# Performance work log

Hardware: AMD Instinct MI355X
Metric: run time of the kernel (lower is better)

## Reference

```python
import jax, jax.numpy as jnp
import numpy as np

N, M, H, C = 20000, 20000, 32, 128
KP_EXTENT = 0.6
EPS = 1e-5


def _kpconv(q_pts, s_pts, neighb_inds, x, kernel_points, weights):
    """Rigid KPConv, linear influence, 'sum' aggregation, Predator-style density norm."""
    # shadow point / shadow feature padding (index M is the shadow slot)
    s_pad = jnp.concatenate([s_pts, jnp.full((1, 3), 1e6, s_pts.dtype)], axis=0)
    x_pad = jnp.concatenate([x, jnp.zeros((1, x.shape[1]), x.dtype)], axis=0)
    neighbors = s_pad[neighb_inds] - q_pts[:, None, :]              # [N,H,3]
    diff = neighbors[:, :, None, :] - kernel_points[None, None]      # [N,H,K,3]
    sq = jnp.sum(diff * diff, axis=-1)                               # [N,H,K]
    dist = jnp.sqrt(jnp.maximum(sq, 1e-12))
    all_weights = jnp.clip(1.0 - dist / KP_EXTENT, 0.0, None)        # linear KP influence
    neighb_x = x_pad[neighb_inds]                                    # [N,H,C]
    weighted = jnp.einsum('nhk,nhc->nkc', all_weights, neighb_x)     # [N,K,C]
    out = jnp.einsum('nkc,kcd->nd', weighted, weights)               # [N,D]
    # density normalization by number of valid neighbors
    feat_sum = jnp.sum(neighb_x, axis=-1)                            # [N,H]
    n_num = jnp.maximum(jnp.sum(feat_sum > 0.0, axis=-1), 1)         # [N]
    return out / n_num[:, None].astype(out.dtype)


def _segment_norm(x, len0):
    """Per-cloud (instance) normalization over stacked points, 2 clouds, no affine."""
    n = x.shape[0]
    seg = (jnp.arange(n) >= len0).astype(jnp.int32)                  # [N] in {0,1}
    onehot = jax.nn.one_hot(seg, 2, dtype=x.dtype)                   # [N,2]
    cnt = jnp.maximum(onehot.sum(axis=0), 1.0)                       # [2]
    mean = (onehot.T @ x) / cnt[:, None]                             # [2,C]
    var = (onehot.T @ (x * x)) / cnt[:, None] - mean * mean          # [2,C]
    return (x - mean[seg]) * jax.lax.rsqrt(var[seg] + EPS)


def _batchnorm1d(x, gamma, beta):
    mean = jnp.mean(x, axis=0)
    var = jnp.mean(x * x, axis=0) - mean * mean                      # biased, as torch BN
    return (x - mean) * jax.lax.rsqrt(var + EPS) * gamma + beta


def _rand_kernel_points(key, k, radius):
    pts = jax.random.normal(key, (k, 3), dtype=jnp.float32)
    pts = pts / jnp.linalg.norm(pts, axis=1, keepdims=True)
    r = jax.random.uniform(jax.random.fold_in(key, 1), (k, 1)) ** (1.0 / 3.0)
    return pts * r * radius


def setup_inputs() -> dict:
    key = jax.random.key(0)
    ks = jax.random.split(key, 10)
    D = C // 2  # 64, per-branch out channels
    q_pts = jax.random.uniform(ks[0], (N, 3), dtype=jnp.float32)
    s_pts = jax.random.uniform(ks[1], (M, 3), dtype=jnp.float32)
    neighb_inds = jax.random.randint(ks[2], (N, H), 0, M)
    x = jax.random.normal(ks[3], (M, C), dtype=jnp.float32)
    stack_lengths_post = jnp.array([N // 2, N - N // 2], dtype=jnp.int32)
    kp_mini = _rand_kernel_points(ks[4], 7, 1.0 * 1.5)               # radius * 1.5
    w_mini = jax.random.normal(ks[5], (7, C, D), dtype=jnp.float32) * (1.0 / np.sqrt(C))
    kp_mid = _rand_kernel_points(ks[6], 13, 1.0)                      # radius
    w_mid = jax.random.normal(ks[7], (13, C, D), dtype=jnp.float32) * (1.0 / np.sqrt(C))
    w_midmini = jax.random.normal(ks[8], (D, D), dtype=jnp.float32) * (1.0 / np.sqrt(D))
    w_final = jax.random.normal(ks[9], (C, C), dtype=jnp.float32) * (1.0 / np.sqrt(C))
    gamma_final = jnp.ones((C,), jnp.float32)
    beta_final = jnp.zeros((C,), jnp.float32)
    return dict(q_pts=q_pts, s_pts=s_pts, neighb_inds=neighb_inds, x=x,
                stack_lengths_post=stack_lengths_post,
                kp_mini=kp_mini, w_mini=w_mini, kp_mid=kp_mid, w_mid=w_mid,
                w_midmini=w_midmini, w_final=w_final,
                gamma_final=gamma_final, beta_final=beta_final)


def reference(q_pts, s_pts, neighb_inds, x, stack_lengths_post,
              kp_mini, w_mini, kp_mid, w_mid, w_midmini, w_final,
              gamma_final, beta_final):
    len0 = stack_lengths_post[0]
    x1 = _kpconv(q_pts, s_pts, neighb_inds, x, kp_mini, w_mini)      # [N, C//2]
    x1 = _segment_norm(x1, len0)
    x2 = _kpconv(q_pts, s_pts, neighb_inds, x, kp_mid, w_mid)        # [N, C//2]
    x2 = _segment_norm(x2, len0)
    x2 = (x1 + x2) @ w_midmini.T                                     # nn.Linear(bias=False)
    xc = jnp.concatenate([x1, x2], axis=1)                           # [N, C]
    out = xc @ w_final.T
    out = _batchnorm1d(out, gamma_final, beta_final)
    return jax.nn.relu(out)
```

## Files before the change

### kernel.cpp

```cpp
#include <hip/hip_runtime.h>
#include <math.h>

#define NQ 20000
#define MS 20000
#define HN 32
#define CH 128
#define DH 64
#define KTOT 20
#define KMINI 7
#define EPSN 1e-5f
#define KDIM 2560
#define NKT 80
#define NMT 1250
#define KT_Y1 28

#define OFF_ROWSUM 0
#define OFF_Y1     20480
#define OFF_Y2     (OFF_Y1 + NQ*DH)
#define OFF_SEG    (OFF_Y2 + NQ*DH)
#define OFF_SEGSUM (OFF_SEG + 512)
#define OFF_BNSUM  (OFF_SEGSUM + 512)
#define OFF_BNSQ   (OFF_BNSUM + 128)
#define OFF_OUTPRE (OFF_BNSQ + 128)
#define OFF_WSWZ   (OFF_OUTPRE + NQ*CH)
#define OFF_P      (OFF_WSWZ + 163840)
#define OFF_CFRAG  (OFF_P + NQ*KDIM/2)
#define TOT_FLOATS (OFF_CFRAG + 8192)

typedef __attribute__((ext_vector_type(8))) short bf16x8;
typedef __attribute__((ext_vector_type(4))) float f32x4;
typedef __attribute__((ext_vector_type(4))) unsigned short us4;

static __device__ inline unsigned short f2bf(float f) {
    unsigned int u = __float_as_uint(f);
    unsigned int r = (u + 0x7fffu + ((u >> 16) & 1u)) >> 16;
    return (unsigned short)r;
}

__global__ __launch_bounds__(256) void k_prep(
    const float* __restrict__ x, float* __restrict__ rowsum,
    const float* __restrict__ w_mini, const float* __restrict__ w_mid,
    const float* __restrict__ w_midmini, const float* __restrict__ w_final,
    unsigned short* __restrict__ wswz, unsigned short* __restrict__ cfrag)
{
    if (blockIdx.x < 5000) {
        int row = blockIdx.x * 4 + (threadIdx.x >> 6);
        int lane = threadIdx.x & 63;
        if (row >= MS) return;
        double s = (double)x[row * CH + lane] + (double)x[row * CH + 64 + lane];
        #pragma unroll
        for (int off = 32; off > 0; off >>= 1) s += __shfl_down(s, off, 64);
        if (lane == 0) rowsum[row] = (float)s;
    } else if (blockIdx.x < 6280) {
        int gid = (blockIdx.x - 5000) * 256 + threadIdx.x;
        if (gid >= NKT * 8 * 512) return;
        int j = gid & 7;
        int l = (gid >> 3) & 63;
        int ntkt = gid >> 9;
        int nt = ntkt & 7;
        int kt = ntkt >> 3;
        int kg = kt * 32 + ((l >> 4) << 3) + j;
        int d  = nt * 16 + (l & 15);
        int k = kg >> 7, c = kg & 127;
        float v = 0.0f;
        if (k < KMINI && d < DH)        v = w_mini[((size_t)k * CH + c) * DH + d];
        else if (k >= KMINI && d >= DH) v = w_mid[((size_t)(k - KMINI) * CH + c) * DH + (d - DH)];
        wswz[gid] = f2bf(v);
    } else {
        int b2 = blockIdx.x - 6280;
        int kt = b2 >> 3, nt = b2 & 7;
        for (int e = threadIdx.x; e < 512; e += 256) {
            int l = e >> 3, j = e & 7;
            int i = kt * 32 + ((l >> 4) << 3) + j;
            int jcol = nt * 16 + (l & 15);
            const float* wfr = &w_final[(size_t)jcol * 128 + 64];
            int ec = i & 63;
            float dsum = 0.f;
            #pragma unroll 8
            for (int dd = 0; dd < 64; ++dd)
                dsum += w_midmini[dd * 64 + ec] * wfr[dd];
            float cv = dsum + ((i < 64) ? w_final[(size_t)jcol * 128 + i] : 0.f);
            cfrag[(size_t)(kt * 8 + nt) * 512 + e] = f2bf(cv);
        }
    }
}

__global__ __launch_bounds__(256) void k_gather(
    const float* __restrict__ q_pts, const float* __restrict__ s_pts,
    const int* __restrict__ inds, const float* __restrict__ x,
    const float* __restrict__ kp_mini, const float* __restrict__ kp_mid,
    const float* __restrict__ rowsum,
    unsigned short* __restrict__ P)
{
    __shared__ __align__(16) float kpts[KTOT][3];
    __shared__ __align__(16) float nb[256][3];
    __shared__ int   nidx[256];
    __shared__ int   vcnt[8];
    __shared__ float winv[8];
    __shared__ __align__(16) float wts[8][HN][KTOT];

    const int t = threadIdx.x;
    const int n0 = blockIdx.x * 8;

    if (t < KTOT * 3) {
        int k = t / 3, j = t % 3;
        kpts[k][j] = (k < KMINI) ? kp_mini[k * 3 + j] : kp_mid[(k - KMINI) * 3 + j];
    }
    if (t < 8) vcnt[t] = 0;
    __syncthreads();

    {
        int r = t >> 5, h = t & 31;
        int n = n0 + r;
        int idx = inds[n * HN + h];
        nidx[t] = idx;
        float qx = q_pts[n * 3 + 0], qy = q_pts[n * 3 + 1], qz = q_pts[n * 3 + 2];
        nb[t][0] = s_pts[idx * 3 + 0] - qx;
        nb[t][1] = s_pts[idx * 3 + 1] - qy;
        nb[t][2] = s_pts[idx * 3 + 2] - qz;
        if (rowsum[idx] > 0.0f) atomicAdd(&vcnt[r], 1);
    }
    __syncthreads();
    if (t < 8) winv[t] = 1.0f / (float)max(vcnt[t], 1);
    __syncthreads();

    for (int tt = t; tt < 8 * HN * KTOT; tt += 256) {
        int r = tt / (HN * KTOT);
        int rem = tt % (HN * KTOT);
        int h = rem / KTOT, k = rem % KTOT;
        float dx = nb[r * HN + h][0] - kpts[k][0];
        float dy = nb[r * HN + h][1] - kpts[k][1];
        float dz = nb[r * HN + h][2] - kpts[k][2];
        float sq = dx * dx + dy * dy + dz * dz;
        float dist = sqrtf(fmaxf(sq, 1e-12f));
        float w = fmaxf(1.0f - dist * (1.0f / 0.6f), 0.0f);
        wts[r][h][k] = w * winv[r];
    }
    __syncthreads();

    const int r = t >> 5;
    const int c4 = t & 31;
    float acc[KTOT][4];
    #pragma unroll
    for (int k = 0; k < KTOT; ++k) {
        acc[k][0] = 0.f; acc[k][1] = 0.f; acc[k][2] = 0.f; acc[k][3] = 0.f;
    }
    const float* wbase = &wts[r][0][0];
    const int* nid = &nidx[r * HN];
    #pragma unroll 2
    for (int h = 0; h < HN; ++h) {
        int idx = nid[h];
        float4 xv = *(const float4*)&x[(size_t)idx * CH + c4 * 4];
        const float4* wp = (const float4*)(wbase + h * KTOT);
        float warr[20];
        *(float4*)&warr[0]  = wp[0];
        *(float4*)&warr[4]  = wp[1];
        *(float4*)&warr[8]  = wp[2];
        *(float4*)&warr[12] = wp[3];
        *(float4*)&warr[16] = wp[4];
        #pragma unroll
        for (int k = 0; k < KTOT; ++k) {
            float wv = warr[k];
            acc[k][0] += wv * xv.x; acc[k][1] += wv * xv.y;
            acc[k][2] += wv * xv.z; acc[k][3] += wv * xv.w;
        }
    }
    const int n = n0 + r;
    const int mt = n >> 4, m15 = n & 15;
    const int lq = (c4 & 7) >> 1;
    const int l = lq * 16 + m15;
    const int j = (c4 & 1) * 4;
    #pragma unroll
    for (int k = 0; k < KTOT; ++k) {
        int kt = k * 4 + (c4 >> 3);
        us4 v;
        v[0] = f2bf(acc[k][0]); v[1] = f2bf(acc[k][1]);
        v[2] = f2bf(acc[k][2]); v[3] = f2bf(acc[k][3]);
        *(us4*)(P + ((size_t)mt * NKT + kt) * 512 + l * 8 + j) = v;
    }
}

__global__ __launch_bounds__(256) void k_mfma(
    const unsigned short* __restrict__ P, const unsigned short* __restrict__ wswz,
    const int* __restrict__ stacklen,
    float* __restrict__ y1, float* __restrict__ y2, float* __restrict__ segsum)
{
    const int t = threadIdx.x;
    const int l = t & 63;
    const int w = t >> 6;
    const int chunk = blockIdx.y;
    const int mtb = blockIdx.x * 8 + w * 2;
    if (mtb >= NMT) return;
    const int kb = chunk ? KT_Y1 : 0;
    const int ke = chunk ? NKT : KT_Y1;
    const int ntb = chunk ? 4 : 0;

    f32x4 acc[2][4];
    #pragma unroll
    for (int i = 0; i < 2; ++i)
        #pragma unroll
        for (int q = 0; q < 4; ++q) acc[i][q] = (f32x4){0.f, 0.f, 0.f, 0.f};

    const size_t astride = (size_t)NKT * 512;
    const unsigned short* a0p = P + (size_t)mtb * astride + l * 8;
    const unsigned short* a1p = (mtb + 1 < NMT) ? a0p + astride : a0p;
    const unsigned short* bp = wswz + l * 8;

    #pragma unroll 2
    for (int kt = kb; kt < ke; ++kt) {
        bf16x8 a0 = *(const bf16x8*)(a0p + (size_t)kt * 512);
        bf16x8 a1 = *(const bf16x8*)(a1p + (size_t)kt * 512);
        #pragma unroll
        for (int q = 0; q < 4; ++q) {
            bf16x8 b = *(const bf16x8*)(bp + (size_t)((kt * 8) + ntb + q) * 512);
            acc[0][q] = __builtin_amdgcn_mfma_f32_16x16x32_bf16(a0, b, acc[0][q], 0, 0, 0);
            acc[1][q] = __builtin_amdgcn_mfma_f32_16x16x32_bf16(a1, b, acc[1][q], 0, 0, 0);
        }
    }

    const int len0 = stacklen[0];
    float* yb = chunk ? y2 : y1;
    const int quad = l >> 4, c16 = l & 15;
    const int base_sum = (chunk * 2) * 2 * 64;

    #pragma unroll
    for (int i = 0; i < 2; ++i) {
        int mt = mtb + i;
        if (mt >= NMT) break;
        bool all0 = (mt * 16 + 15 < len0);
        bool all1 = (mt * 16 >= len0);
        #pragma unroll
        for (int q = 0; q < 4; ++q) {
            float s0 = 0.f, q0 = 0.f, s1 = 0.f, q1 = 0.f;
            #pragma unroll
            for (int reg = 0; reg < 4; ++reg) {
                int row = mt * 16 + quad * 4 + reg;
                float v = acc[i][q][reg];
                yb[(size_t)row * DH + q * 16 + c16] = v;
                if (row < len0) { s0 += v; q0 += v * v; }
                else            { s1 += v; q1 += v * v; }
            }
            s0 += __shfl_xor(s0, 16); s0 += __shfl_xor(s0, 32);
            q0 += __shfl_xor(q0, 16); q0 += __shfl_xor(q0, 32);
            s1 += __shfl_xor(s1, 16); s1 += __shfl_xor(s1, 32);
            q1 += __shfl_xor(q1, 16); q1 += __shfl_xor(q1, 32);
            if (quad == 0) {
                int ch = q * 16 + c16;
                if (!all1) {
                    atomicAdd(&segsum[base_sum + 0 * 64 + ch], s0);
                    atomicAdd(&segsum[base_sum + 1 * 64 + ch], q0);
                }
                if (!all0) {
                    atomicAdd(&segsum[base_sum + 2 * 64 + ch], s1);
                    atomicAdd(&segsum[base_sum + 3 * 64 + ch], q1);
                }
            }
        }
    }
}

__global__ __launch_bounds__(256) void k_tailmm(
    const float* __restrict__ y1, const float* __restrict__ y2,
    const float* __restrict__ segsum, const int* __restrict__ stacklen,
    const unsigned short* __restrict__ cfrag,
    float* __restrict__ outpre, float* __restrict__ bnsum, float* __restrict__ bnsq)
{
    __shared__ __align__(16) unsigned short alds[64 * 136];
    __shared__ float sstat[4][2][64];
    const int t = threadIdx.x;
    const int mb = blockIdx.x * 64;
    const int len0 = stacklen[0];

    {
        int combo = t >> 6, ch = t & 63;
        float cnt = (float)max((combo & 1) ? (NQ - len0) : len0, 1);
        float S = segsum[(combo * 2 + 0) * 64 + ch];
        float Q = segsum[(combo * 2 + 1) * 64 + ch];
        float mean = S / cnt;
        float var = Q / cnt - mean * mean;
        sstat[combo][0][ch] = mean;
        sstat[combo][1][ch] = rsqrtf(fmaxf(var, 0.f) + EPSN);
    }
    __syncthreads();

    for (int tt = t; tt < 64 * 32; tt += 256) {
        int r = tt >> 5, c4 = tt & 31;
        int n = mb + r;
        us4 v4 = (us4){0, 0, 0, 0};
        if (n < NQ) {
            int s = (n >= len0) ? 1 : 0;
            int c = c4 * 4;
            if (c < 64) {
                float4 yv = *(const float4*)&y1[(size_t)n * DH + c];
                v4[0] = f2bf((yv.x - sstat[s][0][c + 0]) * sstat[s][1][c + 0]);
                v4[1] = f2bf((yv.y - sstat[s][0][c + 1]) * sstat[s][1][c + 1]);
                v4[2] = f2bf((yv.z - sstat[s][0][c + 2]) * sstat[s][1][c + 2]);
                v4[3] = f2bf((yv.w - sstat[s][0][c + 3]) * sstat[s][1][c + 3]);
            } else {
                int c2 = c - 64;
                float4 yv = *(const float4*)&y2[(size_t)n * DH + c2];
                v4[0] = f2bf((yv.x - sstat[2 + s][0][c2 + 0]) * sstat[2 + s][1][c2 + 0]);
                v4[1] = f2bf((yv.y - sstat[2 + s][0][c2 + 1]) * sstat[2 + s][1][c2 + 1]);
                v4[2] = f2bf((yv.z - sstat[2 + s][0][c2 + 2]) * sstat[2 + s][1][c2 + 2]);
                v4[3] = f2bf((yv.w - sstat[2 + s][0][c2 + 3]) * sstat[2 + s][1][c2 + 3]);
            }
        }
        *(us4*)(alds + r * 136 + c4 * 4) = v4;
    }
    __syncthreads();

    const int l = t & 63, w = t >> 6;
    f32x4 acc[8];
    #pragma unroll
    for (int q = 0; q < 8; ++q) acc[q] = (f32x4){0.f, 0.f, 0.f, 0.f};

    const unsigned short* ap = alds + (w * 16 + (l & 15)) * 136 + ((l >> 4) << 3);
    const unsigned short* bp = cfrag + l * 8;
    #pragma unroll
    for (int kt = 0; kt < 4; ++kt) {
        bf16x8 a = *(const bf16x8*)(ap + kt * 32);
        #pragma unroll
        for (int nt = 0; nt < 8; ++nt) {
            bf16x8 b = *(const bf16x8*)(bp + (size_t)((kt * 8 + nt) << 9));
            acc[nt] = __builtin_amdgcn_mfma_f32_16x16x32_bf16(a, b, acc[nt], 0, 0, 0);
        }
    }

    const int quad = l >> 4, c16 = l & 15;
    #pragma unroll
    for (int nt = 0; nt < 8; ++nt) {
        float s = 0.f, q = 0.f;
        #pragma unroll
        for (int reg = 0; reg < 4; ++reg) {
            int row = mb + w * 16 + quad * 4 + reg;
            float v = acc[nt][reg];
            if (row < NQ) outpre[(size_t)row * CH + nt * 16 + c16] = v;
            else v = 0.f;
            s += v; q += v * v;
        }
        s += __shfl_xor(s, 16); s += __shfl_xor(s, 32);
        q += __shfl_xor(q, 16); q += __shfl_xor(q, 32);
        if (quad == 0) {
            atomicAdd(&bnsum[nt * 16 + c16], s);
            atomicAdd(&bnsq[nt * 16 + c16], q);
        }
    }
}

__global__ __launch_bounds__(256) void k_kpconv(
    const float* __restrict__ q_pts, const float* __restrict__ s_pts,
    const int* __restrict__ inds, const float* __restrict__ x,
    const float* __restrict__ kp_mini, const float* __restrict__ kp_mid,
    const float* __restrict__ w_mini, const float* __restrict__ w_mid,
    const float* __restrict__ rowsum,
    float* __restrict__ y1, float* __restrict__ y2)
{
    __shared__ __align__(16) float kpts[KTOT][3];
    __shared__ __align__(16) float nb[128][3];
    __shared__ int   nidx[128];
    __shared__ int   vcnt[4];
    __shared__ float winv[4];
    __shared__ __align__(16) float wts[4][HN][KTOT];
    __shared__ __align__(16) float wt[KTOT][CH][4];
    __shared__ __align__(16) float part[128][4];

    const int t = threadIdx.x;
    const int n0 = blockIdx.x * 4;

    if (t < KTOT * 3) {
        int k = t / 3, j = t % 3;
        kpts[k][j] = (k < KMINI) ? kp_mini[k * 3 + j] : kp_mid[(k - KMINI) * 3 + j];
    }
    if (t < 4) vcnt[t] = 0;
    __syncthreads();

    if (t < 128) {
        int r = t >> 5, h = t & 31;
        int n = n0 + r;
        int idx = inds[n * HN + h];
        nidx[t] = idx;
        float qx = q_pts[n * 3 + 0], qy = q_pts[n * 3 + 1], qz = q_pts[n * 3 + 2];
        nb[t][0] = s_pts[idx * 3 + 0] - qx;
        nb[t][1] = s_pts[idx * 3 + 1] - qy;
        nb[t][2] = s_pts[idx * 3 + 2] - qz;
        if (rowsum[idx] > 0.0f) atomicAdd(&vcnt[r], 1);
    }
    __syncthreads();
    if (t < 4) winv[t] = 1.0f / (float)max(vcnt[t], 1);
    __syncthreads();

    for (int tt = t; tt < 4 * HN * KTOT; tt += 256) {
        int r = tt / (HN * KTOT);
        int rem = tt % (HN * KTOT);
        int h = rem / KTOT, k = rem % KTOT;
        float dx = nb[r * HN + h][0] - kpts[k][0];
        float dy = nb[r * HN + h][1] - kpts[k][1];
        float dz = nb[r * HN + h][2] - kpts[k][2];
        float sq = dx * dx + dy * dy + dz * dz;
        float dist = sqrtf(fmaxf(sq, 1e-12f));
        float w = fmaxf(1.0f - dist * (1.0f / 0.6f), 0.0f);
        wts[r][h][k] = w * winv[r];
    }
    __syncthreads();

    {
        const int g = t >> 7;
        const int c = t & 127;
        for (int rr = 0; rr < 2; ++rr) {
            const int r = g + rr * 2;
            float acc[KTOT];
            #pragma unroll
            for (int k = 0; k < KTOT; ++k) acc[k] = 0.0f;
            for (int h = 0; h < HN; ++h) {
                int idx = nidx[r * HN + h];
                float xv = x[(size_t)idx * CH + c];
                const float4* wp = (const float4*)&wts[r][h][0];
                float4 wa = wp[0], wb = wp[1], wc = wp[2], wd = wp[3], we = wp[4];
                acc[0]  += wa.x * xv; acc[1]  += wa.y * xv; acc[2]  += wa.z * xv; acc[3]  += wa.w * xv;
                acc[4]  += wb.x * xv; acc[5]  += wb.y * xv; acc[6]  += wb.z * xv; acc[7]  += wb.w * xv;
                acc[8]  += wc.x * xv; acc[9]  += wc.y * xv; acc[10] += wc.z * xv; acc[11] += wc.w * xv;
                acc[12] += wd.x * xv; acc[13] += wd.y * xv; acc[14] += wd.z * xv; acc[15] += wd.w * xv;
                acc[16] += we.x * xv; acc[17] += we.y * xv; acc[18] += we.z * xv; acc[19] += we.w * xv;
            }
            #pragma unroll
            for (int k = 0; k < KTOT; ++k) wt[k][c][r] = acc[k];
        }
    }
    __syncthreads();

    {
        const int d = t & 127;
        const int half = t >> 7;
        const int c0 = half * 64;
        float o0 = 0.f, o1 = 0.f, o2 = 0.f, o3 = 0.f;
        if (d < DH) {
            for (int k = 0; k < KMINI; ++k) {
                const float* wp = &w_mini[((size_t)k * CH + c0) * DH + d];
                for (int c = c0; c < c0 + 64; ++c) {
                    float wv = *wp; wp += DH;
                    const float4 wtv = *(const float4*)&wt[k][c][0];
                    o0 += wv * wtv.x; o1 += wv * wtv.y; o2 += wv * wtv.z; o3 += wv * wtv.w;
                }
            }
        } else {
            const int dd = d - DH;
            for (int k = KMINI; k < KTOT; ++k) {
                const float* wp = &w_mid[((size_t)(k - KMINI) * CH + c0) * DH + dd];
                for (int c = c0; c < c0 + 64; ++c) {
                    float wv = *wp; wp += DH;
                    const float4 wtv = *(const float4*)&wt[k][c][0];
                    o0 += wv * wtv.x; o1 += wv * wtv.y; o2 += wv * wtv.z; o3 += wv * wtv.w;
                }
            }
        }
        if (half == 1) { part[d][0] = o0; part[d][1] = o1; part[d][2] = o2; part[d][3] = o3; }
        __syncthreads();
        if (half == 0) {
            o0 += part[d][0]; o1 += part[d][1]; o2 += part[d][2]; o3 += part[d][3];
            if (d < DH) {
                y1[(size_t)(n0 + 0) * DH + d] = o0;
                y1[(size_t)(n0 + 1) * DH + d] = o1;
                y1[(size_t)(n0 + 2) * DH + d] = o2;
                y1[(size_t)(n0 + 3) * DH + d] = o3;
            } else {
                const int dd = d - DH;
                y2[(size_t)(n0 + 0) * DH + dd] = o0;
                y2[(size_t)(n0 + 1) * DH + dd] = o1;
                y2[(size_t)(n0 + 2) * DH + dd] = o2;
                y2[(size_t)(n0 + 3) * DH + dd] = o3;
            }
        }
    }
}

__global__ __launch_bounds__(256) void k_segpart(
    const float* __restrict__ y1, const float* __restrict__ y2,
    const int* __restrict__ stacklen, float* __restrict__ segsum)
{
    const int t = threadIdx.x;
    const int ch = t & 63, grp = t >> 6;
    const int len0 = stacklen[0];
    float a0 = 0.f, a1 = 0.f, a2 = 0.f, a3 = 0.f;
    float b0 = 0.f, b1 = 0.f, b2 = 0.f, b3 = 0.f;
    for (int r = blockIdx.x * 4 + grp; r < NQ; r += 256 * 4) {
        float v1 = y1[(size_t)r * DH + ch];
        float v2 = y2[(size_t)r * DH + ch];
        bool in1 = (r >= len0);
        float m0 = in1 ? 0.f : 1.f, m1 = 1.f - m0;
        a0 += m0 * v1; a1 += m0 * v1 * v1; a2 += m1 * v1; a3 += m1 * v1 * v1;
        b0 += m0 * v2; b1 += m0 * v2 * v2; b2 += m1 * v2; b3 += m1 * v2 * v2;
    }
    __shared__ float red[4][8][64];
    red[grp][0][ch] = a0; red[grp][1][ch] = a1; red[grp][2][ch] = a2; red[grp][3][ch] = a3;
    red[grp][4][ch] = b0; red[grp][5][ch] = b1; red[grp][6][ch] = b2; red[grp][7][ch] = b3;
    __syncthreads();
    for (int tt = t; tt < 512; tt += 256) {
        int j = tt >> 6, c = tt & 63;
        float s = red[0][j][c] + red[1][j][c] + red[2][j][c] + red[3][j][c];
        atomicAdd(&segsum[j * 64 + c], s);
    }
}

__global__ __launch_bounds__(256) void k_tail(
    const float* __restrict__ y1, const float* __restrict__ y2,
    const float* __restrict__ segsum, const int* __restrict__ stacklen,
    const float* __restrict__ w_midmini, const float* __restrict__ w_final,
    float* __restrict__ outpre, float* __restrict__ bnsum, float* __restrict__ bnsq)
{
    __shared__ __align__(16) float sstat[4][2][64];
    __shared__ __align__(16) float sbuf[8][64];
    __shared__ __align__(16) float xc[8][128];
    __shared__ float lsum[2][128], lsq[2][128];
    const int n0 = blockIdx.x * 8;
    const int t = threadIdx.x;
    const int len0 = stacklen[0];

    {
        int combo = t >> 6, ch = t & 63;
        float cnt = (float)max((combo & 1) ? (NQ - len0) : len0, 1);
        float S = segsum[(combo * 2 + 0) * 64 + ch];
        float Q = segsum[(combo * 2 + 1) * 64 + ch];
        float mean = S / cnt;
        float var = Q / cnt - mean * mean;
        sstat[combo][0][ch] = mean;
        sstat[combo][1][ch] = rsqrtf(fmaxf(var, 0.f) + EPSN);
    }
    __syncthreads();

    for (int tt = t; tt < 8 * 64; tt += 256) {
        int r = tt >> 6, d = tt & 63;
        int n = n0 + r;
        int s = (n >= len0) ? 1 : 0;
        float x1n = (y1[(size_t)n * DH + d] - sstat[s][0][d]) * sstat[s][1][d];
        float x2n = (y2[(size_t)n * DH + d] - sstat[2 + s][0][d]) * sstat[2 + s][1][d];
        xc[r][d] = x1n;
        sbuf[r][d] = x1n + x2n;
    }
    __syncthreads();

    for (int tt = t; tt < 8 * 64; tt += 256) {
        int r = tt >> 6, d = tt & 63;
        float a = 0.f;
        const float4* wmr = (const float4*)&w_midmini[(size_t)d * 64];
        const float4* sv = (const float4*)&sbuf[r][0];
        #pragma unroll
        for (int e4 = 0; e4 < 16; ++e4) {
            float4 w4 = wmr[e4], s4 = sv[e4];
            a += w4.x * s4.x + w4.y * s4.y + w4.z * s4.z + w4.w * s4.w;
        }
        xc[r][64 + d] = a;
    }
    __syncthreads();

    {
        const int j = t & 127;
        const int g = t >> 7;
        float o0 = 0.f, o1 = 0.f, o2 = 0.f, o3 = 0.f;
        const float4* wfr = (const float4*)&w_final[(size_t)j * 128];
        #pragma unroll 8
        for (int i4 = 0; i4 < 32; ++i4) {
            float4 wf = wfr[i4];
            float4 a0 = *(const float4*)&xc[g + 0][i4 * 4];
            float4 a1 = *(const float4*)&xc[g + 2][i4 * 4];
            float4 a2 = *(const float4*)&xc[g + 4][i4 * 4];
            float4 a3 = *(const float4*)&xc[g + 6][i4 * 4];
            o0 += wf.x * a0.x + wf.y * a0.y + wf.z * a0.z + wf.w * a0.w;
            o1 += wf.x * a1.x + wf.y * a1.y + wf.z * a1.z + wf.w * a1.w;
            o2 += wf.x * a2.x + wf.y * a2.y + wf.z * a2.z + wf.w * a2.w;
            o3 += wf.x * a3.x + wf.y * a3.y + wf.z * a3.z + wf.w * a3.w;
        }
        outpre[(size_t)(n0 + g + 0) * CH + j] = o0;
        outpre[(size_t)(n0 + g + 2) * CH + j] = o1;
        outpre[(size_t)(n0 + g + 4) * CH + j] = o2;
        outpre[(size_t)(n0 + g + 6) * CH + j] = o3;
        lsum[g][j] = o0 + o1 + o2 + o3;
        lsq[g][j]  = o0 * o0 + o1 * o1 + o2 * o2 + o3 * o3;
        __syncthreads();
        if (g == 0) {
            atomicAdd(&bnsum[j], lsum[0][j] + lsum[1][j]);
            atomicAdd(&bnsq[j],  lsq[0][j] + lsq[1][j]);
        }
    }
}

__global__ __launch_bounds__(256) void k_bnapply(const float* __restrict__ outpre,
    const float* __restrict__ bnsum, const float* __restrict__ bnsq,
    const float* __restrict__ gamma, const float* __restrict__ beta,
    float* __restrict__ out)
{
    int e4 = blockIdx.x * 256 + threadIdx.x;
    if (e4 >= NQ * CH / 4) return;
    int j0 = (e4 * 4) & 127;
    float4 v = ((const float4*)outpre)[e4];
    float vv[4] = {v.x, v.y, v.z, v.w};
    float res[4];
    #pragma unroll
    for (int i = 0; i < 4; ++i) {
        int j = j0 + i;
        float mean = bnsum[j] * (1.0f / NQ);
        float var = bnsq[j] * (1.0f / NQ) - mean * mean;
        float rstd = rsqrtf(fmaxf(var, 0.f) + EPSN);
        float r = (vv[i] - mean) * rstd * gamma[j] + beta[j];
        res[i] = fmaxf(r, 0.f);
    }
    ((float4*)out)[e4] = make_float4(res[0], res[1], res[2], res[3]);
}

extern "C" void kernel_launch(void* const* d_in, const int* in_sizes, int n_in,
                              void* d_out, int out_size, void* d_ws, size_t ws_size,
                              hipStream_t stream) {
    const float* q_pts     = (const float*)d_in[0];
    const float* s_pts     = (const float*)d_in[1];
    const int*   inds      = (const int*)d_in[2];
    const float* x         = (const float*)d_in[3];
    const int*   stacklen  = (const int*)d_in[4];
    const float* kp_mini   = (const float*)d_in[5];
    const float* w_mini    = (const float*)d_in[6];
    const float* kp_mid    = (const float*)d_in[7];
    const float* w_mid     = (const float*)d_in[8];
    const float* w_midmini = (const float*)d_in[9];
    const float* w_final   = (const float*)d_in[10];
    const float* gamma     = (const float*)d_in[11];
    const float* beta      = (const float*)d_in[12];

    float* ws      = (float*)d_ws;
    float* rowsum  = ws + OFF_ROWSUM;
    float* y1      = ws + OFF_Y1;
    float* y2      = ws + OFF_Y2;
    float* segsum  = ws + OFF_SEGSUM;
    float* bnsum   = ws + OFF_BNSUM;
    float* bnsq    = ws + OFF_BNSQ;
    float* outpre  = ws + OFF_OUTPRE;
    unsigned short* wswz  = (unsigned short*)(ws + OFF_WSWZ);
    unsigned short* P     = (unsigned short*)(ws + OFF_P);
    unsigned short* cfrag = (unsigned short*)(ws + OFF_CFRAG);

    hipMemsetAsync(segsum, 0, 768 * sizeof(float), stream);

    if (ws_size >= (size_t)TOT_FLOATS * sizeof(float)) {
        k_prep<<<5000 + 1280 + 32, 256, 0, stream>>>(x, rowsum, w_mini, w_mid,
                                                     w_midmini, w_final, wswz, cfrag);
        k_gather<<<NQ / 8, 256, 0, stream>>>(q_pts, s_pts, inds, x, kp_mini, kp_mid,
                                             rowsum, P);
        dim3 mg((NMT + 7) / 8, 2);
        k_mfma<<<mg, 256, 0, stream>>>(P, wswz, stacklen, y1, y2, segsum);
        k_tailmm<<<(NQ + 63) / 64, 256, 0, stream>>>(y1, y2, segsum, stacklen, cfrag,
                                                     outpre, bnsum, bnsq);
    } else {
        k_prep<<<5000, 256, 0, stream>>>(x, rowsum, w_mini, w_mid,
                                         w_midmini, w_final, wswz, cfrag);
        k_kpconv<<<NQ / 4, 256, 0, stream>>>(q_pts, s_pts, inds, x, kp_mini, kp_mid,
                                             w_mini, w_mid, rowsum, y1, y2);
        k_segpart<<<256, 256, 0, stream>>>(y1, y2, stacklen, segsum);
        k_tail<<<NQ / 8, 256, 0, stream>>>(y1, y2, segsum, stacklen, w_midmini, w_final,
                                           outpre, bnsum, bnsq);
    }

    k_bnapply<<<(NQ * CH / 4 + 255) / 256, 256, 0, stream>>>(outpre, bnsum, bnsq,
                                                             gamma, beta, (float*)d_out);
}
```

Baseline: 263.0 us.

## Fuse gather and MFMA kernels, keep P in LDS, gather bf16 features

Merges the gather kernel and the MFMA GEMM kernel into one kernel per 16 query points. The per-point kernel-weighted features P are now computed with MFMA from a gathered bf16 x tile and kept in shared memory, so the large P round trip through global memory goes away. The prep kernel also writes a bf16 copy of x to halve gather traffic, and its rowsum step is restructured to 16 rows per block. In exchange the fused kernel uses about 140KB of LDS, which allows only one block per CU, the K-split needs a cross-wave reduction, and rounding x and the weights to bf16 earlier adds some error.

```diff
diff --git a/kernel.cpp b/kernel.cpp
--- a/kernel.cpp
+++ b/kernel.cpp
@@ -9,27 +9,25 @@
 #define KTOT 20
 #define KMINI 7
 #define EPSN 1e-5f
-#define KDIM 2560
 #define NKT 80
-#define NMT 1250
 #define KT_Y1 28
 
 #define OFF_ROWSUM 0
 #define OFF_Y1     20480
 #define OFF_Y2     (OFF_Y1 + NQ*DH)
-#define OFF_SEG    (OFF_Y2 + NQ*DH)
-#define OFF_SEGSUM (OFF_SEG + 512)
+#define OFF_SEGSUM (OFF_Y2 + NQ*DH)
 #define OFF_BNSUM  (OFF_SEGSUM + 512)
 #define OFF_BNSQ   (OFF_BNSUM + 128)
 #define OFF_OUTPRE (OFF_BNSQ + 128)
 #define OFF_WSWZ   (OFF_OUTPRE + NQ*CH)
-#define OFF_P      (OFF_WSWZ + 163840)
-#define OFF_CFRAG  (OFF_P + NQ*KDIM/2)
-#define TOT_FLOATS (OFF_CFRAG + 8192)
+#define OFF_CFRAG  (OFF_WSWZ + 163840)
+#define OFF_XBF    (OFF_CFRAG + 8192)
+#define TOT_FLOATS (OFF_XBF + NQ*CH/2)
 
 typedef __attribute__((ext_vector_type(8))) short bf16x8;
 typedef __attribute__((ext_vector_type(4))) float f32x4;
 typedef __attribute__((ext_vector_type(4))) unsigned short us4;
+typedef __attribute__((ext_vector_type(8))) unsigned short us8;
 
 static __device__ inline unsigned short f2bf(float f) {
     unsigned int u = __float_as_uint(f);
@@ -41,18 +39,27 @@
     const float* __restrict__ x, float* __restrict__ rowsum,
     const float* __restrict__ w_mini, const float* __restrict__ w_mid,
     const float* __restrict__ w_midmini, const float* __restrict__ w_final,
-    unsigned short* __restrict__ wswz, unsigned short* __restrict__ cfrag)
+    unsigned short* __restrict__ wswz, unsigned short* __restrict__ cfrag,
+    unsigned short* __restrict__ x_bf)
 {
-    if (blockIdx.x < 5000) {
-        int row = blockIdx.x * 4 + (threadIdx.x >> 6);
-        int lane = threadIdx.x & 63;
-        if (row >= MS) return;
-        double s = (double)x[row * CH + lane] + (double)x[row * CH + 64 + lane];
-        #pragma unroll
-        for (int off = 32; off > 0; off >>= 1) s += __shfl_down(s, off, 64);
-        if (lane == 0) rowsum[row] = (float)s;
-    } else if (blockIdx.x < 6280) {
-        int gid = (blockIdx.x - 5000) * 256 + threadIdx.x;
+    const int t = threadIdx.x;
+    if (blockIdx.x < 1250) {
+        int row = blockIdx.x * 16 + (t >> 4);
+        int l16 = t & 15;
+        const float4* xr = (const float4*)&x[(size_t)row * CH + l16 * 8];
+        float4 a = xr[0], b = xr[1];
+        if (x_bf) {
+            us8 v;
+            v[0] = f2bf(a.x); v[1] = f2bf(a.y); v[2] = f2bf(a.z); v[3] = f2bf(a.w);
+            v[4] = f2bf(b.x); v[5] = f2bf(b.y); v[6] = f2bf(b.z); v[7] = f2bf(b.w);
+            *(us8*)&x_bf[(size_t)row * CH + l16 * 8] = v;
+        }
+        double s = (double)a.x + a.y + a.z + a.w + b.x + b.y + b.z + b.w;
+        #pragma unroll
+        for (int off = 8; off > 0; off >>= 1) s += __shfl_down(s, off, 64);
+        if (l16 == 0) rowsum[row] = (float)s;
+    } else if (blockIdx.x < 2530) {
+        int gid = (blockIdx.x - 1250) * 256 + t;
         if (gid >= NKT * 8 * 512) return;
         int j = gid & 7;
         int l = (gid >> 3) & 63;
@@ -67,9 +74,9 @@
         else if (k >= KMINI && d >= DH) v = w_mid[((size_t)(k - KMINI) * CH + c) * DH + (d - DH)];
         wswz[gid] = f2bf(v);
     } else {
-        int b2 = blockIdx.x - 6280;
+        int b2 = blockIdx.x - 2530;
         int kt = b2 >> 3, nt = b2 & 7;
-        for (int e = threadIdx.x; e < 512; e += 256) {
+        for (int e = t; e < 512; e += 256) {
             int l = e >> 3, j = e & 7;
             int i = kt * 32 + ((l >> 4) << 3) + j;
             int jcol = nt * 16 + (l & 15);
@@ -85,158 +92,153 @@
     }
 }
 
-__global__ __launch_bounds__(256) void k_gather(
+__global__ __launch_bounds__(256) void k_fused(
     const float* __restrict__ q_pts, const float* __restrict__ s_pts,
-    const int* __restrict__ inds, const float* __restrict__ x,
+    const int* __restrict__ inds, const unsigned short* __restrict__ x_bf,
     const float* __restrict__ kp_mini, const float* __restrict__ kp_mid,
-    const float* __restrict__ rowsum,
-    unsigned short* __restrict__ P)
+    const float* __restrict__ rowsum, const unsigned short* __restrict__ wswz,
+    const int* __restrict__ stacklen,
+    float* __restrict__ y1, float* __restrict__ y2, float* __restrict__ segsum)
 {
-    __shared__ __align__(16) float kpts[KTOT][3];
-    __shared__ __align__(16) float nb[256][3];
-    __shared__ int   nidx[256];
-    __shared__ int   vcnt[8];
-    __shared__ float winv[8];
-    __shared__ __align__(16) float wts[8][HN][KTOT];
+    __shared__ __align__(16) char pool[142592];
+    unsigned short* Pt  = (unsigned short*)pool;
+    unsigned short* wts = (unsigned short*)(pool + 82176);
+    float*          red = (float*)(pool + 82176);
+    unsigned short* xg  = (unsigned short*)(pool + 107776);
+    float*          nbv = (float*)(pool + 107776);
+    __shared__ int nidx[512];
+    __shared__ float kpts[KTOT][3];
+    __shared__ int vcnt[16];
+    __shared__ float winv[16];
 
     const int t = threadIdx.x;
-    const int n0 = blockIdx.x * 8;
+    const int l = t & 63;
+    const int w = t >> 6;
+    const int n0 = blockIdx.x * 16;
+    const int c16 = l & 15;
+    const int rq = l >> 4;
 
     if (t < KTOT * 3) {
         int k = t / 3, j = t % 3;
         kpts[k][j] = (k < KMINI) ? kp_mini[k * 3 + j] : kp_mid[(k - KMINI) * 3 + j];
     }
-    if (t < 8) vcnt[t] = 0;
-    __syncthreads();
-
-    {
-        int r = t >> 5, h = t & 31;
+    if (t < 16) vcnt[t] = 0;
+    __syncthreads();
+
+    for (int tt = t; tt < 512; tt += 256) {
+        int r = tt >> 5, h = tt & 31;
         int n = n0 + r;
         int idx = inds[n * HN + h];
-        nidx[t] = idx;
+        nidx[tt] = idx;
         float qx = q_pts[n * 3 + 0], qy = q_pts[n * 3 + 1], qz = q_pts[n * 3 + 2];
-        nb[t][0] = s_pts[idx * 3 + 0] - qx;
-        nb[t][1] = s_pts[idx * 3 + 1] - qy;
-        nb[t][2] = s_pts[idx * 3 + 2] - qz;
+        nbv[tt * 3 + 0] = s_pts[idx * 3 + 0] - qx;
+        nbv[tt * 3 + 1] = s_pts[idx * 3 + 1] - qy;
+        nbv[tt * 3 + 2] = s_pts[idx * 3 + 2] - qz;
         if (rowsum[idx] > 0.0f) atomicAdd(&vcnt[r], 1);
     }
     __syncthreads();
-    if (t < 8) winv[t] = 1.0f / (float)max(vcnt[t], 1);
-    __syncthreads();
-
-    for (int tt = t; tt < 8 * HN * KTOT; tt += 256) {
+    if (t < 16) winv[t] = 1.0f / (float)max(vcnt[t], 1);
+    __syncthreads();
+
+    for (int tt = t; tt < 16 * HN * KTOT; tt += 256) {
         int r = tt / (HN * KTOT);
         int rem = tt % (HN * KTOT);
         int h = rem / KTOT, k = rem % KTOT;
-        float dx = nb[r * HN + h][0] - kpts[k][0];
-        float dy = nb[r * HN + h][1] - kpts[k][1];
-        float dz = nb[r * HN + h][2] - kpts[k][2];
+        float dx = nbv[(r * HN + h) * 3 + 0] - kpts[k][0];
+        float dy = nbv[(r * HN + h) * 3 + 1] - kpts[k][1];
+        float dz = nbv[(r * HN + h) * 3 + 2] - kpts[k][2];
         float sq = dx * dx + dy * dy + dz * dz;
         float dist = sqrtf(fmaxf(sq, 1e-12f));
-        float w = fmaxf(1.0f - dist * (1.0f / 0.6f), 0.0f);
-        wts[r][h][k] = w * winv[r];
-    }
-    __syncthreads();
-
-    const int r = t >> 5;
-    const int c4 = t & 31;
-    float acc[KTOT][4];
+        float wv = fmaxf(1.0f - dist * (1.0f / 0.6f), 0.0f);
+        wts[(r * KTOT + k) * 40 + h] = f2bf(wv * winv[r]);
+    }
+    __syncthreads();
+
+    unsigned short* myxg = xg + w * (HN * 136);
+    for (int step = 0; step < 4; ++step) {
+        const int r = w * 4 + step;
+        #pragma unroll
+        for (int i = 0; i < 8; ++i) {
+            int h = i * 4 + rq;
+            int idx = nidx[r * HN + h];
+            us8 v = *(const us8*)&x_bf[(size_t)idx * CH + c16 * 8];
+            *(us8*)&myxg[h * 136 + c16 * 8] = v;
+        }
+        bf16x8 a0 = *(const bf16x8*)&wts[(r * KTOT + c16) * 40 + rq * 8];
+        bf16x8 a1 = *(const bf16x8*)&wts[(r * KTOT + 16 + c16) * 40 + rq * 8];
+        f32x4 pa0[8], pa1[8];
+        #pragma unroll
+        for (int nt = 0; nt < 8; ++nt) { pa0[nt] = (f32x4){0.f,0.f,0.f,0.f}; pa1[nt] = (f32x4){0.f,0.f,0.f,0.f}; }
+        #pragma unroll
+        for (int nt = 0; nt < 8; ++nt) {
+            bf16x8 bb;
+            #pragma unroll
+            for (int j = 0; j < 8; ++j)
+                bb[j] = (short)myxg[(rq * 8 + j) * 136 + nt * 16 + c16];
+            pa0[nt] = __builtin_amdgcn_mfma_f32_16x16x32_bf16(a0, bb, pa0[nt], 0, 0, 0);
+            pa1[nt] = __builtin_amdgcn_mfma_f32_16x16x32_bf16(a1, bb, pa1[nt], 0, 0, 0);
+        }
+        #pragma unroll
+        for (int nt = 0; nt < 8; ++nt) {
+            int c = nt * 16 + c16;
+            #pragma unroll
+            for (int reg = 0; reg < 4; ++reg) {
+                Pt[r * 2568 + (rq * 4 + reg) * 128 + c] = f2bf(pa0[nt][reg]);
+            }
+            if (rq == 0) {
+                #pragma unroll
+                for (int reg = 0; reg < 4; ++reg)
+                    Pt[r * 2568 + (16 + reg) * 128 + c] = f2bf(pa1[nt][reg]);
+            }
+        }
+    }
+    __syncthreads();
+
+    f32x4 macc[8];
     #pragma unroll
-    for (int k = 0; k < KTOT; ++k) {
-        acc[k][0] = 0.f; acc[k][1] = 0.f; acc[k][2] = 0.f; acc[k][3] = 0.f;
-    }
-    const float* wbase = &wts[r][0][0];
-    const int* nid = &nidx[r * HN];
-    #pragma unroll 2
-    for (int h = 0; h < HN; ++h) {
-        int idx = nid[h];
-        float4 xv = *(const float4*)&x[(size_t)idx * CH + c4 * 4];
-        const float4* wp = (const float4*)(wbase + h * KTOT);
-        float warr[20];
-        *(float4*)&warr[0]  = wp[0];
-        *(float4*)&warr[4]  = wp[1];
-        *(float4*)&warr[8]  = wp[2];
-        *(float4*)&warr[12] = wp[3];
-        *(float4*)&warr[16] = wp[4];
-        #pragma unroll
-        for (int k = 0; k < KTOT; ++k) {
-            float wv = warr[k];
-            acc[k][0] += wv * xv.x; acc[k][1] += wv * xv.y;
-            acc[k][2] += wv * xv.z; acc[k][3] += wv * xv.w;
-        }
-    }
-    const int n = n0 + r;
-    const int mt = n >> 4, m15 = n & 15;
-    const int lq = (c4 & 7) >> 1;
-    const int l = lq * 16 + m15;
-    const int j = (c4 & 1) * 4;
-    #pragma unroll
-    for (int k = 0; k < KTOT; ++k) {
-        int kt = k * 4 + (c4 >> 3);
-        us4 v;
-        v[0] = f2bf(acc[k][0]); v[1] = f2bf(acc[k][1]);
-        v[2] = f2bf(acc[k][2]); v[3] = f2bf(acc[k][3]);
-        *(us4*)(P + ((size_t)mt * NKT + kt) * 512 + l * 8 + j) = v;
-    }
-}
-
-__global__ __launch_bounds__(256) void k_mfma(
-    const unsigned short* __restrict__ P, const unsigned short* __restrict__ wswz,
-    const int* __restrict__ stacklen,
-    float* __restrict__ y1, float* __restrict__ y2, float* __restrict__ segsum)
-{
-    const int t = threadIdx.x;
-    const int l = t & 63;
-    const int w = t >> 6;
-    const int chunk = blockIdx.y;
-    const int mtb = blockIdx.x * 8 + w * 2;
-    if (mtb >= NMT) return;
-    const int kb = chunk ? KT_Y1 : 0;
-    const int ke = chunk ? NKT : KT_Y1;
-    const int ntb = chunk ? 4 : 0;
-
-    f32x4 acc[2][4];
-    #pragma unroll
-    for (int i = 0; i < 2; ++i)
-        #pragma unroll
-        for (int q = 0; q < 4; ++q) acc[i][q] = (f32x4){0.f, 0.f, 0.f, 0.f};
-
-    const size_t astride = (size_t)NKT * 512;
-    const unsigned short* a0p = P + (size_t)mtb * astride + l * 8;
-    const unsigned short* a1p = (mtb + 1 < NMT) ? a0p + astride : a0p;
-    const unsigned short* bp = wswz + l * 8;
-
-    #pragma unroll 2
-    for (int kt = kb; kt < ke; ++kt) {
-        bf16x8 a0 = *(const bf16x8*)(a0p + (size_t)kt * 512);
-        bf16x8 a1 = *(const bf16x8*)(a1p + (size_t)kt * 512);
+    for (int q = 0; q < 8; ++q) macc[q] = (f32x4){0.f, 0.f, 0.f, 0.f};
+    const int ktb = w * 20;
+    for (int kt = ktb; kt < ktb + 20; ++kt) {
+        bf16x8 a = *(const bf16x8*)&Pt[c16 * 2568 + kt * 32 + rq * 8];
+        const int ntb = (kt < KT_Y1) ? 0 : 4;
         #pragma unroll
         for (int q = 0; q < 4; ++q) {
-            bf16x8 b = *(const bf16x8*)(bp + (size_t)((kt * 8) + ntb + q) * 512);
-            acc[0][q] = __builtin_amdgcn_mfma_f32_16x16x32_bf16(a0, b, acc[0][q], 0, 0, 0);
-            acc[1][q] = __builtin_amdgcn_mfma_f32_16x16x32_bf16(a1, b, acc[1][q], 0, 0, 0);
-        }
-    }
-
-    const int len0 = stacklen[0];
-    float* yb = chunk ? y2 : y1;
-    const int quad = l >> 4, c16 = l & 15;
-    const int base_sum = (chunk * 2) * 2 * 64;
-
-    #pragma unroll
-    for (int i = 0; i < 2; ++i) {
-        int mt = mtb + i;
-        if (mt >= NMT) break;
-        bool all0 = (mt * 16 + 15 < len0);
-        bool all1 = (mt * 16 >= len0);
-        #pragma unroll
-        for (int q = 0; q < 4; ++q) {
+            bf16x8 b = *(const bf16x8*)&wswz[(size_t)(kt * 8 + ntb + q) * 512 + l * 8];
+            macc[ntb + q] = __builtin_amdgcn_mfma_f32_16x16x32_bf16(a, b, macc[ntb + q], 0, 0, 0);
+        }
+    }
+
+    if (w > 0) {
+        float* rp = red + ((w - 1) * 64 + l) * 33;
+        #pragma unroll
+        for (int q = 0; q < 8; ++q)
+            #pragma unroll
+            for (int reg = 0; reg < 4; ++reg) rp[q * 4 + reg] = macc[q][reg];
+    }
+    __syncthreads();
+    if (w == 0) {
+        #pragma unroll
+        for (int i = 0; i < 3; ++i) {
+            const float* rp = red + (i * 64 + l) * 33;
+            #pragma unroll
+            for (int q = 0; q < 8; ++q)
+                #pragma unroll
+                for (int reg = 0; reg < 4; ++reg) macc[q][reg] += rp[q * 4 + reg];
+        }
+        const int len0 = stacklen[0];
+        bool allseg0 = (n0 + 15 < len0);
+        bool allseg1 = (n0 >= len0);
+        #pragma unroll
+        for (int nt = 0; nt < 8; ++nt) {
+            float* yb = (nt < 4) ? y1 : y2;
+            int col = (nt & 3) * 16 + c16;
+            int sbase = (nt < 4) ? 0 : 256;
             float s0 = 0.f, q0 = 0.f, s1 = 0.f, q1 = 0.f;
             #pragma unroll
             for (int reg = 0; reg < 4; ++reg) {
-                int row = mt * 16 + quad * 4 + reg;
-                float v = acc[i][q][reg];
-                yb[(size_t)row * DH + q * 16 + c16] = v;
+                int row = n0 + rq * 4 + reg;
+                float v = macc[nt][reg];
+                yb[(size_t)row * DH + col] = v;
                 if (row < len0) { s0 += v; q0 += v * v; }
                 else            { s1 += v; q1 += v * v; }
             }
@@ -244,15 +246,14 @@
             q0 += __shfl_xor(q0, 16); q0 += __shfl_xor(q0, 32);
             s1 += __shfl_xor(s1, 16); s1 += __shfl_xor(s1, 32);
             q1 += __shfl_xor(q1, 16); q1 += __shfl_xor(q1, 32);
-            if (quad == 0) {
-                int ch = q * 16 + c16;
-                if (!all1) {
-                    atomicAdd(&segsum[base_sum + 0 * 64 + ch], s0);
-                    atomicAdd(&segsum[base_sum + 1 * 64 + ch], q0);
+            if (rq == 0) {
+                if (!allseg1) {
+                    atomicAdd(&segsum[sbase + 0 * 64 + col], s0);
+                    atomicAdd(&segsum[sbase + 1 * 64 + col], q0);
                 }
-                if (!all0) {
-                    atomicAdd(&segsum[base_sum + 2 * 64 + ch], s1);
-                    atomicAdd(&segsum[base_sum + 3 * 64 + ch], q1);
+                if (!allseg0) {
+                    atomicAdd(&segsum[sbase + 2 * 64 + col], s1);
+                    atomicAdd(&segsum[sbase + 3 * 64 + col], q1);
                 }
             }
         }
@@ -632,23 +633,21 @@
     float* bnsq    = ws + OFF_BNSQ;
     float* outpre  = ws + OFF_OUTPRE;
     unsigned short* wswz  = (unsigned short*)(ws + OFF_WSWZ);
-    unsigned short* P     = (unsigned short*)(ws + OFF_P);
     unsigned short* cfrag = (unsigned short*)(ws + OFF_CFRAG);
+    unsigned short* x_bf  = (unsigned short*)(ws + OFF_XBF);
 
     hipMemsetAsync(segsum, 0, 768 * sizeof(float), stream);
 
     if (ws_size >= (size_t)TOT_FLOATS * sizeof(float)) {
-        k_prep<<<5000 + 1280 + 32, 256, 0, stream>>>(x, rowsum, w_mini, w_mid,
-                                                     w_midmini, w_final, wswz, cfrag);
-        k_gather<<<NQ / 8, 256, 0, stream>>>(q_pts, s_pts, inds, x, kp_mini, kp_mid,
-                                             rowsum, P);
-        dim3 mg((NMT + 7) / 8, 2);
-        k_mfma<<<mg, 256, 0, stream>>>(P, wswz, stacklen, y1, y2, segsum);
+        k_prep<<<1250 + 1280 + 32, 256, 0, stream>>>(x, rowsum, w_mini, w_mid,
+                                                     w_midmini, w_final, wswz, cfrag, x_bf);
+        k_fused<<<1250, 256, 0, stream>>>(q_pts, s_pts, inds, x_bf, kp_mini, kp_mid,
+                                          rowsum, wswz, stacklen, y1, y2, segsum);
         k_tailmm<<<(NQ + 63) / 64, 256, 0, stream>>>(y1, y2, segsum, stacklen, cfrag,
                                                      outpre, bnsum, bnsq);
     } else {
-        k_prep<<<5000, 256, 0, stream>>>(x, rowsum, w_mini, w_mid,
-                                         w_midmini, w_final, wswz, cfrag);
+        k_prep<<<1250, 256, 0, stream>>>(x, rowsum, w_mini, w_mid,
+                                         w_midmini, w_final, wswz, cfrag, (unsigned short*)0);
         k_kpconv<<<NQ / 4, 256, 0, stream>>>(q_pts, s_pts, inds, x, kp_mini, kp_mid,
                                              w_mini, w_mid, rowsum, y1, y2);
         k_segpart<<<256, 256, 0, stream>>>(y1, y2, stacklen, segsum);
```

After: 981.0 us. +272.9%, slower.
